# Kernel tuning notes

Measured on AMD Instinct MI355X. Metric: run time of the kernel, lower is better.

Reference implementation:

```python
import jax, jax.numpy as jnp
import numpy as np

B, S, D, H, DK, DV, L = 2, 2048, 256, 8, 32, 32, 3


def positional_encoding(seq_len, d_model):
    pos = jnp.arange(seq_len, dtype=jnp.float32)[:, None]
    div = jnp.exp(jnp.arange(0, d_model, 2, dtype=jnp.float32) * (-np.log(10000.0) / d_model))
    pe = jnp.zeros((seq_len, d_model), jnp.float32)
    pe = pe.at[:, 0::2].set(jnp.sin(pos * div))
    pe = pe.at[:, 1::2].set(jnp.cos(pos * div))
    return pe  # [S, D]


def setup_inputs() -> dict:
    key = jax.random.key(0)
    ks = jax.random.split(key, 5)
    w_scale = 1.0 / np.sqrt(D)
    return {
        "seq_inputs": jax.random.normal(ks[0], (B, S, D), dtype=jnp.float32),
        "Wq": jax.random.normal(ks[1], (L, D, H * DK), dtype=jnp.float32) * w_scale,
        "Wk": jax.random.normal(ks[2], (L, D, H * DK), dtype=jnp.float32) * w_scale,
        "Wv": jax.random.normal(ks[3], (L, D, H * DV), dtype=jnp.float32) * w_scale,
        "Wfc": jax.random.normal(ks[4], (L, H * DV, D), dtype=jnp.float32) * w_scale,
    }


def reference(seq_inputs, Wq, Wk, Wv, Wfc):
    # positional encoding add (dropout is identity in eval)
    x = seq_inputs + positional_encoding(S, D)[None]  # [B,S,D]
    inv_sqrt_dk = 1.0 / np.sqrt(DK)

    def layer(x, w):
        wq, wk, wv, wfc = w
        q = (x @ wq).reshape(B, S, H, DK).transpose(0, 2, 1, 3)  # [B,H,S,DK]
        k = (x @ wk).reshape(B, S, H, DK).transpose(0, 2, 1, 3)
        v = (x @ wv).reshape(B, S, H, DV).transpose(0, 2, 1, 3)
        scores = jnp.einsum('bhqd,bhkd->bhqk', q, k) * inv_sqrt_dk  # [B,H,S,S]
        attn = jax.nn.softmax(scores, axis=-1)
        ctx = jnp.einsum('bhqk,bhkd->bhqd', attn, v)  # [B,H,S,DV]
        ctx = ctx.transpose(0, 2, 1, 3).reshape(B, S, H * DV)
        # NOTE: original torch code has NO residual add and NO layernorm applied
        return ctx @ wfc, attn

    out, attns = jax.lax.scan(layer, x, (Wq, Wk, Wv, Wfc))
    return out, attns  # out: [B,S,D], attns: [L,B,H,S,S]
```

## Files before the change

kernel.cpp:

```cpp
#include <hip/hip_runtime.h>
#include <hip/hip_bf16.h>

#define BB 2
#define SS 2048
#define DD 256
#define HH 8
#define DKK 32
#define DVV 32
#define LL 3

typedef __hip_bfloat16 bf16;
typedef __attribute__((ext_vector_type(8))) short bfrag;
typedef __attribute__((ext_vector_type(4))) float f4;

__device__ __forceinline__ bfrag ld8(const bf16* p) {
  return *reinterpret_cast<const bfrag*>(p);
}

__global__ __launch_bounds__(256) void cast_weights_k(const float* __restrict__ wq,
                                                      const float* __restrict__ wk,
                                                      const float* __restrict__ wv,
                                                      const float* __restrict__ wfc,
                                                      bf16* __restrict__ wts) {
  int e = blockIdx.x * 256 + threadIdx.x;
  int mat = e >> 16;
  int t = mat & 3;
  int l = mat >> 2;
  int kk = (e >> 8) & 255;
  int n = e & 255;
  const float* src = (t == 0) ? wq : (t == 1) ? wk : (t == 2) ? wv : wfc;
  float v = src[((size_t)l * 256 + kk) * 256 + n];
  wts[(size_t)mat * 65536 + (size_t)n * 256 + kk] = __float2bfloat16(v);
}

__global__ __launch_bounds__(256) void pe_add_k(const float* __restrict__ seq,
                                                bf16* __restrict__ xbf) {
  int e = blockIdx.x * 256 + threadIdx.x;
  int d = e & 255;
  int m = e >> 8;
  int s = m & (SS - 1);
  int i2 = d >> 1;
  float div = __expf((float)(2 * i2) * (-9.210340371976184f / 256.0f));
  float ang = (float)s * div;
  float pe = (d & 1) ? __cosf(ang) : __sinf(ang);
  xbf[e] = __float2bfloat16(seq[e] + pe);
}

__global__ __launch_bounds__(256) void proj_k(const bf16* __restrict__ xbf,
                                              const bf16* __restrict__ wl,
                                              bf16* __restrict__ q,
                                              bf16* __restrict__ k,
                                              bf16* __restrict__ vt) {
  int lane = threadIdx.x & 63;
  int wv = threadIdx.x >> 6;
  int c = lane & 15, g = lane >> 4;
  int t = blockIdx.y >> 2;
  int n0 = (blockIdx.y & 3) * 64;
  int m0 = blockIdx.x * 64 + wv * 16;
  const bf16* wt = wl + (size_t)t * 65536;
  const bf16* arow = xbf + (size_t)(m0 + c) * 256 + g * 8;
  f4 acc[4];
#pragma unroll
  for (int i = 0; i < 4; ++i) acc[i] = (f4){0.f, 0.f, 0.f, 0.f};
#pragma unroll
  for (int kk = 0; kk < 8; ++kk) {
    bfrag af = ld8(arow + kk * 32);
#pragma unroll
    for (int ns = 0; ns < 4; ++ns) {
      bfrag bfr = ld8(wt + (size_t)(n0 + ns * 16 + c) * 256 + kk * 32 + g * 8);
      acc[ns] = __builtin_amdgcn_mfma_f32_16x16x32_bf16(af, bfr, acc[ns], 0, 0, 0);
    }
  }
#pragma unroll
  for (int ns = 0; ns < 4; ++ns) {
#pragma unroll
    for (int r = 0; r < 4; ++r) {
      int m = m0 + g * 4 + r;
      int n = n0 + ns * 16 + c;
      int b = m >> 11, s = m & (SS - 1);
      int h = n >> 5, d = n & 31;
      bf16 v = __float2bfloat16(acc[ns][r]);
      if (t == 0)      q[((size_t)(b * HH + h) * SS + s) * DKK + d] = v;
      else if (t == 1) k[((size_t)(b * HH + h) * SS + s) * DKK + d] = v;
      else             vt[((size_t)(b * HH + h) * DVV + d) * SS + s] = v;
    }
  }
}

__global__ __launch_bounds__(256) void fc_k(const bf16* __restrict__ ctxbf,
                                            const bf16* __restrict__ wt,
                                            bf16* __restrict__ xbf,
                                            float* __restrict__ fout, int wf) {
  int lane = threadIdx.x & 63;
  int wv = threadIdx.x >> 6;
  int c = lane & 15, g = lane >> 4;
  int n0 = blockIdx.y * 64;
  int m0 = blockIdx.x * 64 + wv * 16;
  const bf16* arow = ctxbf + (size_t)(m0 + c) * 256 + g * 8;
  f4 acc[4];
#pragma unroll
  for (int i = 0; i < 4; ++i) acc[i] = (f4){0.f, 0.f, 0.f, 0.f};
#pragma unroll
  for (int kk = 0; kk < 8; ++kk) {
    bfrag af = ld8(arow + kk * 32);
#pragma unroll
    for (int ns = 0; ns < 4; ++ns) {
      bfrag bfr = ld8(wt + (size_t)(n0 + ns * 16 + c) * 256 + kk * 32 + g * 8);
      acc[ns] = __builtin_amdgcn_mfma_f32_16x16x32_bf16(af, bfr, acc[ns], 0, 0, 0);
    }
  }
#pragma unroll
  for (int ns = 0; ns < 4; ++ns) {
#pragma unroll
    for (int r = 0; r < 4; ++r) {
      int m = m0 + g * 4 + r;
      int n = n0 + ns * 16 + c;
      float v = acc[ns][r];
      xbf[(size_t)m * 256 + n] = __float2bfloat16(v);
      if (wf) fout[(size_t)m * 256 + n] = v;
    }
  }
}

__global__ __launch_bounds__(256) void attn_full_k(const bf16* __restrict__ q,
                                                   const bf16* __restrict__ k,
                                                   const bf16* __restrict__ vt,
                                                   float* __restrict__ aout,
                                                   bf16* __restrict__ ctxbf) {
  const float C2 = 0.2550350812540738f;
  int lane = threadIdx.x & 63;
  int wv = threadIdx.x >> 6;
  int c = lane & 15, g = lane >> 4;
  int bh = blockIdx.y;
  int b = bh >> 3, h = bh & 7;
  int s0 = blockIdx.x * 64 + wv * 16;
  const bf16* qb = q + ((size_t)bh * SS + s0) * DKK;
  const bf16* kb = k + (size_t)bh * SS * DKK;
  const bf16* vb = vt + (size_t)bh * DVV * SS;
  bfrag qf = ld8(qb + c * DKK + g * 8);
  const f4 z = {0.f, 0.f, 0.f, 0.f};

  float sums[4] = {0.f, 0.f, 0.f, 0.f};
#pragma unroll 4
  for (int kc = 0; kc < SS / 16; ++kc) {
    bfrag kf = ld8(kb + (size_t)(kc * 16 + c) * DKK + g * 8);
    f4 sc = __builtin_amdgcn_mfma_f32_16x16x32_bf16(qf, kf, z, 0, 0, 0);
#pragma unroll
    for (int r = 0; r < 4; ++r) sums[r] += __builtin_amdgcn_exp2f(sc[r] * C2);
  }
#pragma unroll
  for (int mm = 1; mm < 16; mm <<= 1) {
#pragma unroll
    for (int r = 0; r < 4; ++r) sums[r] += __shfl_xor(sums[r], mm, 64);
  }
  float invr[4];
#pragma unroll
  for (int r = 0; r < 4; ++r) invr[r] = 1.0f / sums[r];

  __shared__ __align__(16) float pws[4][16 * 64];
  __shared__ __align__(16) bf16 pbf[4][16][40];
  float* pw = pws[wv];
  float* arow = aout + ((size_t)bh * SS + s0) * SS;
  f4 acc0 = z, acc1 = z;

  for (int j = 0; j < SS / 64; ++j) {
#pragma unroll
    for (int half = 0; half < 2; ++half) {
#pragma unroll
      for (int t2 = 0; t2 < 2; ++t2) {
        int t = half * 2 + t2;
        bfrag kf = ld8(kb + (size_t)(j * 64 + t * 16 + c) * DKK + g * 8);
        f4 sc = __builtin_amdgcn_mfma_f32_16x16x32_bf16(qf, kf, z, 0, 0, 0);
#pragma unroll
        for (int r = 0; r < 4; ++r) {
          float p = __builtin_amdgcn_exp2f(sc[r] * C2) * invr[r];
          int row = g * 4 + r;
          int col = t * 16 + c;
          pw[row * 64 + (((col >> 2) ^ row) << 2) + (col & 3)] = p;
          pbf[wv][row][t2 * 16 + c] = __float2bfloat16(p);
        }
      }
      bfrag pa = ld8(&pbf[wv][c][g * 8]);
      bfrag vf0 = ld8(vb + (size_t)c * SS + j * 64 + half * 32 + g * 8);
      acc0 = __builtin_amdgcn_mfma_f32_16x16x32_bf16(pa, vf0, acc0, 0, 0, 0);
      bfrag vf1 = ld8(vb + (size_t)(16 + c) * SS + j * 64 + half * 32 + g * 8);
      acc1 = __builtin_amdgcn_mfma_f32_16x16x32_bf16(pa, vf1, acc1, 0, 0, 0);
    }
#pragma unroll
    for (int qq = 0; qq < 4; ++qq) {
      int row = qq * 4 + g;
      f4 v = *reinterpret_cast<f4*>(&pw[row * 64 + ((c ^ row) << 2)]);
      *reinterpret_cast<f4*>(&arow[(size_t)row * SS + j * 64 + (c << 2)]) = v;
    }
  }

#pragma unroll
  for (int r = 0; r < 4; ++r) {
    int srow = s0 + g * 4 + r;
    size_t base = ((size_t)b * SS + srow) * 256 + h * 32;
    ctxbf[base + c] = __float2bfloat16(acc0[r]);
    ctxbf[base + 16 + c] = __float2bfloat16(acc1[r]);
  }
}

extern "C" void kernel_launch(void* const* d_in, const int* in_sizes, int n_in,
                              void* d_out, int out_size, void* d_ws, size_t ws_size,
                              hipStream_t stream) {
  (void)in_sizes; (void)n_in; (void)out_size; (void)ws_size;
  const float* seq = (const float*)d_in[0];
  const float* Wq  = (const float*)d_in[1];
  const float* Wk  = (const float*)d_in[2];
  const float* Wv  = (const float*)d_in[3];
  const float* Wfc = (const float*)d_in[4];
  float* out = (float*)d_out;
  float* attns = out + (size_t)BB * SS * DD;

  const size_t MB2 = 2097152;
  char* ws = (char*)d_ws;
  bf16* wts  = (bf16*)(ws);
  bf16* xbf  = (bf16*)(ws + 1572864);
  bf16* vtb  = (bf16*)(ws + 1572864 + MB2);
  bf16* ctxb = (bf16*)(ws + 1572864 + 2 * MB2);
  bf16* qb   = (bf16*)(ws + 1572864 + 3 * MB2);
  bf16* kb   = (bf16*)(ws + 1572864 + 4 * MB2);

  cast_weights_k<<<3072, 256, 0, stream>>>(Wq, Wk, Wv, Wfc, wts);
  pe_add_k<<<4096, 256, 0, stream>>>(seq, xbf);

  for (int l = 0; l < LL; ++l) {
    proj_k<<<dim3(64, 12), 256, 0, stream>>>(xbf, wts + (size_t)l * 4 * 65536, qb, kb, vtb);
    attn_full_k<<<dim3(SS / 64, BB * HH), 256, 0, stream>>>(
        qb, kb, vtb, attns + (size_t)l * BB * HH * SS * SS, ctxb);
    fc_k<<<dim3(64, 4), 256, 0, stream>>>(ctxb, wts + ((size_t)l * 4 + 3) * 65536,
                                          xbf, out, (l == LL - 1) ? 1 : 0);
  }
}
```

Before: 344.0 us.

## Software-pipeline attention tile: compute next block's probabilities while storing current

```diff
diff --git a/kernel.cpp b/kernel.cpp
--- a/kernel.cpp
+++ b/kernel.cpp
@@ -157,39 +157,76 @@
 #pragma unroll
   for (int r = 0; r < 4; ++r) invr[r] = 1.0f / sums[r];
 
-  __shared__ __align__(16) float pws[4][16 * 64];
-  __shared__ __align__(16) bf16 pbf[4][16][40];
-  float* pw = pws[wv];
+  __shared__ __align__(16) float pws[4][2][16 * 64];
+  __shared__ __align__(16) bf16 pbf[4][2][16][72];
   float* arow = aout + ((size_t)bh * SS + s0) * SS;
   f4 acc0 = z, acc1 = z;
-
-  for (int j = 0; j < SS / 64; ++j) {
-#pragma unroll
-    for (int half = 0; half < 2; ++half) {
-#pragma unroll
-      for (int t2 = 0; t2 < 2; ++t2) {
-        int t = half * 2 + t2;
-        bfrag kf = ld8(kb + (size_t)(j * 64 + t * 16 + c) * DKK + g * 8);
-        f4 sc = __builtin_amdgcn_mfma_f32_16x16x32_bf16(qf, kf, z, 0, 0, 0);
-#pragma unroll
-        for (int r = 0; r < 4; ++r) {
-          float p = __builtin_amdgcn_exp2f(sc[r] * C2) * invr[r];
-          int row = g * 4 + r;
-          int col = t * 16 + c;
-          pw[row * 64 + (((col >> 2) ^ row) << 2) + (col & 3)] = p;
-          pbf[wv][row][t2 * 16 + c] = __float2bfloat16(p);
-        }
-      }
-      bfrag pa = ld8(&pbf[wv][c][g * 8]);
-      bfrag vf0 = ld8(vb + (size_t)c * SS + j * 64 + half * 32 + g * 8);
+  f4 pv[4];
+
+#pragma unroll
+  for (int t = 0; t < 4; ++t) {
+    bfrag kf = ld8(kb + (size_t)(t * 16 + c) * DKK + g * 8);
+    f4 sc = __builtin_amdgcn_mfma_f32_16x16x32_bf16(qf, kf, z, 0, 0, 0);
+#pragma unroll
+    for (int r = 0; r < 4; ++r) pv[t][r] = __builtin_amdgcn_exp2f(sc[r] * C2) * invr[r];
+  }
+#pragma unroll
+  for (int t = 0; t < 4; ++t) {
+#pragma unroll
+    for (int r = 0; r < 4; ++r) {
+      int row = g * 4 + r, col = t * 16 + c;
+      pws[wv][0][row * 64 + (((col >> 2) ^ row) << 2) + (col & 3)] = pv[t][r];
+      pbf[wv][0][row][col] = __float2bfloat16(pv[t][r]);
+    }
+  }
+
+  for (int j = 0; j < SS / 64 - 1; ++j) {
+    int buf = j & 1;
+#pragma unroll
+    for (int t = 0; t < 4; ++t) {
+      bfrag kf = ld8(kb + (size_t)((j + 1) * 64 + t * 16 + c) * DKK + g * 8);
+      f4 sc = __builtin_amdgcn_mfma_f32_16x16x32_bf16(qf, kf, z, 0, 0, 0);
+#pragma unroll
+      for (int r = 0; r < 4; ++r) pv[t][r] = __builtin_amdgcn_exp2f(sc[r] * C2) * invr[r];
+    }
+#pragma unroll
+    for (int ks = 0; ks < 2; ++ks) {
+      bfrag pa = ld8(&pbf[wv][buf][c][ks * 32 + g * 8]);
+      bfrag vf0 = ld8(vb + (size_t)c * SS + j * 64 + ks * 32 + g * 8);
       acc0 = __builtin_amdgcn_mfma_f32_16x16x32_bf16(pa, vf0, acc0, 0, 0, 0);
-      bfrag vf1 = ld8(vb + (size_t)(16 + c) * SS + j * 64 + half * 32 + g * 8);
+      bfrag vf1 = ld8(vb + (size_t)(16 + c) * SS + j * 64 + ks * 32 + g * 8);
       acc1 = __builtin_amdgcn_mfma_f32_16x16x32_bf16(pa, vf1, acc1, 0, 0, 0);
     }
 #pragma unroll
     for (int qq = 0; qq < 4; ++qq) {
       int row = qq * 4 + g;
-      f4 v = *reinterpret_cast<f4*>(&pw[row * 64 + ((c ^ row) << 2)]);
+      f4 v = *reinterpret_cast<f4*>(&pws[wv][buf][row * 64 + ((c ^ row) << 2)]);
+      *reinterpret_cast<f4*>(&arow[(size_t)row * SS + j * 64 + (c << 2)]) = v;
+    }
+#pragma unroll
+    for (int t = 0; t < 4; ++t) {
+#pragma unroll
+      for (int r = 0; r < 4; ++r) {
+        int row = g * 4 + r, col = t * 16 + c;
+        pws[wv][buf ^ 1][row * 64 + (((col >> 2) ^ row) << 2) + (col & 3)] = pv[t][r];
+        pbf[wv][buf ^ 1][row][col] = __float2bfloat16(pv[t][r]);
+      }
+    }
+  }
+  {
+    int j = SS / 64 - 1, buf = j & 1;
+#pragma unroll
+    for (int ks = 0; ks < 2; ++ks) {
+      bfrag pa = ld8(&pbf[wv][buf][c][ks * 32 + g * 8]);
+      bfrag vf0 = ld8(vb + (size_t)c * SS + j * 64 + ks * 32 + g * 8);
+      acc0 = __builtin_amdgcn_mfma_f32_16x16x32_bf16(pa, vf0, acc0, 0, 0, 0);
+      bfrag vf1 = ld8(vb + (size_t)(16 + c) * SS + j * 64 + ks * 32 + g * 8);
+      acc1 = __builtin_amdgcn_mfma_f32_16x16x32_bf16(pa, vf1, acc1, 0, 0, 0);
+    }
+#pragma unroll
+    for (int qq = 0; qq < 4; ++qq) {
+      int row = qq * 4 + g;
+      f4 v = *reinterpret_cast<f4*>(&pws[wv][buf][row * 64 + ((c ^ row) << 2)]);
       *reinterpret_cast<f4*>(&arow[(size_t)row * SS + j * 64 + (c << 2)]) = v;
     }
   }
```

Measured after the change: 380.2 us. 1.11x slower.

## Process 32 query rows per single-wave attention block to reuse K and V loads

Applied to the files above, without the earlier changes.

```diff
diff --git a/kernel.cpp b/kernel.cpp
--- a/kernel.cpp
+++ b/kernel.cpp
@@ -122,84 +122,111 @@
   }
 }
 
-__global__ __launch_bounds__(256) void attn_full_k(const bf16* __restrict__ q,
-                                                   const bf16* __restrict__ k,
-                                                   const bf16* __restrict__ vt,
-                                                   float* __restrict__ aout,
-                                                   bf16* __restrict__ ctxbf) {
+__global__ __launch_bounds__(64) void attn_full_k(const bf16* __restrict__ q,
+                                                  const bf16* __restrict__ k,
+                                                  const bf16* __restrict__ vt,
+                                                  float* __restrict__ aout,
+                                                  bf16* __restrict__ ctxbf) {
   const float C2 = 0.2550350812540738f;
-  int lane = threadIdx.x & 63;
-  int wv = threadIdx.x >> 6;
+  int lane = threadIdx.x;
   int c = lane & 15, g = lane >> 4;
   int bh = blockIdx.y;
   int b = bh >> 3, h = bh & 7;
-  int s0 = blockIdx.x * 64 + wv * 16;
+  int s0 = blockIdx.x * 32;
   const bf16* qb = q + ((size_t)bh * SS + s0) * DKK;
   const bf16* kb = k + (size_t)bh * SS * DKK;
   const bf16* vb = vt + (size_t)bh * DVV * SS;
-  bfrag qf = ld8(qb + c * DKK + g * 8);
+  bfrag qf0 = ld8(qb + c * DKK + g * 8);
+  bfrag qf1 = ld8(qb + (size_t)(16 + c) * DKK + g * 8);
   const f4 z = {0.f, 0.f, 0.f, 0.f};
 
-  float sums[4] = {0.f, 0.f, 0.f, 0.f};
+  float sums0[4] = {0.f, 0.f, 0.f, 0.f};
+  float sums1[4] = {0.f, 0.f, 0.f, 0.f};
 #pragma unroll 4
   for (int kc = 0; kc < SS / 16; ++kc) {
     bfrag kf = ld8(kb + (size_t)(kc * 16 + c) * DKK + g * 8);
-    f4 sc = __builtin_amdgcn_mfma_f32_16x16x32_bf16(qf, kf, z, 0, 0, 0);
-#pragma unroll
-    for (int r = 0; r < 4; ++r) sums[r] += __builtin_amdgcn_exp2f(sc[r] * C2);
+    f4 sc0 = __builtin_amdgcn_mfma_f32_16x16x32_bf16(qf0, kf, z, 0, 0, 0);
+    f4 sc1 = __builtin_amdgcn_mfma_f32_16x16x32_bf16(qf1, kf, z, 0, 0, 0);
+#pragma unroll
+    for (int r = 0; r < 4; ++r) {
+      sums0[r] += __builtin_amdgcn_exp2f(sc0[r] * C2);
+      sums1[r] += __builtin_amdgcn_exp2f(sc1[r] * C2);
+    }
   }
 #pragma unroll
   for (int mm = 1; mm < 16; mm <<= 1) {
 #pragma unroll
-    for (int r = 0; r < 4; ++r) sums[r] += __shfl_xor(sums[r], mm, 64);
-  }
-  float invr[4];
-#pragma unroll
-  for (int r = 0; r < 4; ++r) invr[r] = 1.0f / sums[r];
-
-  __shared__ __align__(16) float pws[4][16 * 64];
-  __shared__ __align__(16) bf16 pbf[4][16][40];
-  float* pw = pws[wv];
+    for (int r = 0; r < 4; ++r) {
+      sums0[r] += __shfl_xor(sums0[r], mm, 64);
+      sums1[r] += __shfl_xor(sums1[r], mm, 64);
+    }
+  }
+  float inv0[4], inv1[4];
+#pragma unroll
+  for (int r = 0; r < 4; ++r) { inv0[r] = 1.0f / sums0[r]; inv1[r] = 1.0f / sums1[r]; }
+
+  __shared__ __align__(16) float pws[32 * 64];
+  __shared__ __align__(16) bf16 pbf[32][72];
   float* arow = aout + ((size_t)bh * SS + s0) * SS;
-  f4 acc0 = z, acc1 = z;
+  f4 acc0 = z, acc1 = z, acc2 = z, acc3 = z;
 
   for (int j = 0; j < SS / 64; ++j) {
 #pragma unroll
-    for (int half = 0; half < 2; ++half) {
-#pragma unroll
-      for (int t2 = 0; t2 < 2; ++t2) {
-        int t = half * 2 + t2;
-        bfrag kf = ld8(kb + (size_t)(j * 64 + t * 16 + c) * DKK + g * 8);
-        f4 sc = __builtin_amdgcn_mfma_f32_16x16x32_bf16(qf, kf, z, 0, 0, 0);
-#pragma unroll
-        for (int r = 0; r < 4; ++r) {
-          float p = __builtin_amdgcn_exp2f(sc[r] * C2) * invr[r];
+    for (int t = 0; t < 4; ++t) {
+      bfrag kf = ld8(kb + (size_t)(j * 64 + t * 16 + c) * DKK + g * 8);
+      f4 sc0 = __builtin_amdgcn_mfma_f32_16x16x32_bf16(qf0, kf, z, 0, 0, 0);
+      f4 sc1 = __builtin_amdgcn_mfma_f32_16x16x32_bf16(qf1, kf, z, 0, 0, 0);
+#pragma unroll
+      for (int r = 0; r < 4; ++r) {
+        int col = t * 16 + c;
+        int F = col >> 2;
+        {
+          float p = __builtin_amdgcn_exp2f(sc0[r] * C2) * inv0[r];
           int row = g * 4 + r;
-          int col = t * 16 + c;
-          pw[row * 64 + (((col >> 2) ^ row) << 2) + (col & 3)] = p;
-          pbf[wv][row][t2 * 16 + c] = __float2bfloat16(p);
+          pws[row * 64 + ((F ^ row) << 2) + (col & 3)] = p;
+          pbf[row][col] = __float2bfloat16(p);
+        }
+        {
+          float p = __builtin_amdgcn_exp2f(sc1[r] * C2) * inv1[r];
+          int row = 16 + g * 4 + r;
+          pws[row * 64 + ((F ^ (row & 15)) << 2) + (col & 3)] = p;
+          pbf[row][col] = __float2bfloat16(p);
         }
       }
-      bfrag pa = ld8(&pbf[wv][c][g * 8]);
-      bfrag vf0 = ld8(vb + (size_t)c * SS + j * 64 + half * 32 + g * 8);
-      acc0 = __builtin_amdgcn_mfma_f32_16x16x32_bf16(pa, vf0, acc0, 0, 0, 0);
-      bfrag vf1 = ld8(vb + (size_t)(16 + c) * SS + j * 64 + half * 32 + g * 8);
-      acc1 = __builtin_amdgcn_mfma_f32_16x16x32_bf16(pa, vf1, acc1, 0, 0, 0);
-    }
-#pragma unroll
-    for (int qq = 0; qq < 4; ++qq) {
+    }
+#pragma unroll
+    for (int ks = 0; ks < 2; ++ks) {
+      bfrag vf0 = ld8(vb + (size_t)c * SS + j * 64 + ks * 32 + g * 8);
+      bfrag vf1 = ld8(vb + (size_t)(16 + c) * SS + j * 64 + ks * 32 + g * 8);
+      bfrag paL = ld8(&pbf[c][ks * 32 + g * 8]);
+      acc0 = __builtin_amdgcn_mfma_f32_16x16x32_bf16(paL, vf0, acc0, 0, 0, 0);
+      acc1 = __builtin_amdgcn_mfma_f32_16x16x32_bf16(paL, vf1, acc1, 0, 0, 0);
+      bfrag paH = ld8(&pbf[16 + c][ks * 32 + g * 8]);
+      acc2 = __builtin_amdgcn_mfma_f32_16x16x32_bf16(paH, vf0, acc2, 0, 0, 0);
+      acc3 = __builtin_amdgcn_mfma_f32_16x16x32_bf16(paH, vf1, acc3, 0, 0, 0);
+    }
+#pragma unroll
+    for (int qq = 0; qq < 8; ++qq) {
       int row = qq * 4 + g;
-      f4 v = *reinterpret_cast<f4*>(&pw[row * 64 + ((c ^ row) << 2)]);
+      f4 v = *reinterpret_cast<f4*>(&pws[row * 64 + ((c ^ (row & 15)) << 2)]);
       *reinterpret_cast<f4*>(&arow[(size_t)row * SS + j * 64 + (c << 2)]) = v;
     }
   }
 
 #pragma unroll
   for (int r = 0; r < 4; ++r) {
-    int srow = s0 + g * 4 + r;
-    size_t base = ((size_t)b * SS + srow) * 256 + h * 32;
-    ctxbf[base + c] = __float2bfloat16(acc0[r]);
-    ctxbf[base + 16 + c] = __float2bfloat16(acc1[r]);
+    {
+      int srow = s0 + g * 4 + r;
+      size_t base = ((size_t)b * SS + srow) * 256 + h * 32;
+      ctxbf[base + c] = __float2bfloat16(acc0[r]);
+      ctxbf[base + 16 + c] = __float2bfloat16(acc1[r]);
+    }
+    {
+      int srow = s0 + 16 + g * 4 + r;
+      size_t base = ((size_t)b * SS + srow) * 256 + h * 32;
+      ctxbf[base + c] = __float2bfloat16(acc2[r]);
+      ctxbf[base + 16 + c] = __float2bfloat16(acc3[r]);
+    }
   }
 }
 
@@ -229,7 +256,7 @@
 
   for (int l = 0; l < LL; ++l) {
     proj_k<<<dim3(64, 12), 256, 0, stream>>>(xbf, wts + (size_t)l * 4 * 65536, qb, kb, vtb);
-    attn_full_k<<<dim3(SS / 64, BB * HH), 256, 0, stream>>>(
+    attn_full_k<<<dim3(SS / 32, BB * HH), 64, 0, stream>>>(
         qb, kb, vtb, attns + (size_t)l * BB * HH * SS * SS, ctxb);
     fc_k<<<dim3(64, 4), 256, 0, stream>>>(ctxb, wts + ((size_t)l * 4 + 3) * 65536,
                                           xbf, out, (l == LL - 1) ? 1 : 0);
```

After: 457.4 us. 33.0% more time.
